# Kernel optimization log

Hardware: AMD Instinct MI355X
Metric: run time of the kernel (lower is better)

## Reference

```python
import jax, jax.numpy as jnp
import numpy as np

B, CF, HH, WW = 32, 768, 28, 28
M, NH = 32, 1024
BETA = 0.05

def _lin(key, out_d, in_d):
    k1, k2 = jax.random.split(key)
    s = 1.0 / np.sqrt(in_d)
    W = jax.random.uniform(k1, (out_d, in_d), minval=-s, maxval=s, dtype=jnp.float32)
    b = jax.random.uniform(k2, (out_d,), minval=-s, maxval=s, dtype=jnp.float32)
    return W, b

def setup_inputs() -> dict:
    key = jax.random.key(0)
    ks = jax.random.split(key, 16)
    inp = {
        'F': jax.random.normal(ks[0], (B, CF, HH, WW), dtype=jnp.float32),
        'A': jax.random.uniform(ks[1], (B, M, HH, WW), dtype=jnp.float32),
        'C': jax.random.normal(ks[2], (1, M * CF), dtype=jnp.float32),
    }
    names = ['xi', 'hi', 'xf', 'hf', 'xo', 'ho', 'xc', 'hc']
    for i, n in enumerate(names):
        in_d = CF if n[0] == 'x' else NH
        W, b = _lin(ks[3 + i], NH, in_d)
        inp['W' + n] = W
        inp['b' + n] = b
    return inp

def reference(F, A, C, Wxi, bxi, Whi, bhi, Wxf, bxf, Whf, bhf, Wxo, bxo, Who, bho, Wxc, bxc, Whc, bhc):
    b = F.shape[0]
    hw = F.shape[2] * F.shape[3]
    m = A.shape[1]
    # BAP: avg-pool of F * A_i over spatial dims, for each attention map -> [B, M, Cf]
    V = jnp.einsum('bchw,bmhw->bmc', F, A) / hw
    V = V.reshape(b, -1)  # [B, M*Cf]
    # RCLoss (center update + detached MSE)
    tmp = jnp.sum(V - C, axis=0)  # [M*Cf]
    C_new = C + (BETA * tmp / b)[None, :]
    diff = jax.lax.stop_gradient(V) - jax.lax.stop_gradient(C_new)
    rcloss = jnp.mean(diff * diff)
    # LSTM over M steps (note: original uses sigmoid for all gates via Sig_i)
    X_seq = V.reshape(b, m, -1).transpose(1, 0, 2)  # [M, B, Cf]
    h0 = jnp.zeros((b, Whi.shape[0]), dtype=V.dtype)
    c0 = jnp.zeros((b, Whi.shape[0]), dtype=V.dtype)
    def step(carry, X):
        H, Cc = carry
        I = jax.nn.sigmoid(X @ Wxi.T + bxi + H @ Whi.T + bhi)
        Fg = jax.nn.sigmoid(X @ Wxf.T + bxf + H @ Whf.T + bhf)
        O = jax.nn.sigmoid(X @ Wxo.T + bxo + H @ Who.T + bho)
        Ct = jnp.tanh(X @ Wxc.T + bxc + H @ Whc.T + bhc)
        Cc = Fg * Cc + I * Ct
        H = O * jnp.tanh(Cc)
        return (H, Cc), None
    (H, _), _ = jax.lax.scan(step, (h0, c0), X_seq)
    return (H, rcloss, C_new)
```

## Files before the change

### kernel.cpp

```cpp
#include <hip/hip_runtime.h>
#include <math.h>

#define CF 768
#define MM 32
#define HW 784
#define MCF 24576
#define BETA 0.05f

typedef __attribute__((ext_vector_type(8))) short bf16x8;
typedef __attribute__((ext_vector_type(4))) float f32x4;

__device__ __forceinline__ unsigned short bf16rne(float x) {
    unsigned int bits = __float_as_uint(x);
    unsigned int r = (bits + 0x7fffu + ((bits >> 16) & 1u)) >> 16;
    return (unsigned short)r;
}
__device__ __forceinline__ float bf2f(unsigned short u) {
    return __uint_as_float(((unsigned int)u) << 16);
}
__device__ __forceinline__ float sigf(float x) { return 1.f / (1.f + __expf(-x)); }
__device__ __forceinline__ float ftanh(float x) {
    x = fminf(fmaxf(x, -12.f), 12.f);
    float e = __expf(2.f * x);
    return (e - 1.f) / (e + 1.f);
}

__device__ __forceinline__ void cvt8(const float4 a, const float4 b, unsigned short* u) {
    u[0] = bf16rne(a.x); u[1] = bf16rne(a.y); u[2] = bf16rne(a.z); u[3] = bf16rne(a.w);
    u[4] = bf16rne(b.x); u[5] = bf16rne(b.y); u[6] = bf16rne(b.z); u[7] = bf16rne(b.w);
}

__global__ __launch_bounds__(256) void kA3M(
    const float* __restrict__ F, const float* __restrict__ Ain,
    unsigned short* __restrict__ Vbf,
    const float* __restrict__ Wxi, const float* __restrict__ Wxf,
    const float* __restrict__ Wxo, const float* __restrict__ Wxc,
    unsigned short* __restrict__ Wxbf,
    const float* __restrict__ Whi, const float* __restrict__ Whf,
    const float* __restrict__ Who, const float* __restrict__ Whc,
    unsigned short* __restrict__ Wbf,
    float* __restrict__ outRC) {
    __shared__ unsigned short Alds[3328 * 8];
    __shared__ unsigned short Flds[2][512 * 8];
    const int bid = blockIdx.x;
    const int t = threadIdx.x;

    if (bid >= 384) {
        if (bid == 384 && t == 0) outRC[0] = 0.f;
        if (bid < 1920) {
            int gid = (bid - 384) * 256 + t;
            int row = gid / 96;
            int kq = (gid - row * 96) * 8;
            int g = row >> 10, j = row & 1023;
            const float* Wg = (g == 0) ? Wxi : (g == 1) ? Wxf : (g == 2) ? Wxo : Wxc;
            const float* src = Wg + (size_t)j * CF + kq;
            float4 f0 = *(const float4*)src;
            float4 f1 = *(const float4*)(src + 4);
            unsigned short u[8];
            cvt8(f0, f1, u);
            *(uint4*)&Wxbf[(size_t)row * CF + kq] = *(const uint4*)u;
        } else {
            size_t tid8 = ((size_t)(bid - 1920) * 256 + t) * 8;
            int row = (int)(tid8 >> 10);
            int k = (int)(tid8 & 1023);
            int g = row >> 10, j = row & 1023;
            const float* Wg = (g == 0) ? Whi : (g == 1) ? Whf : (g == 2) ? Who : Whc;
            const float* src = Wg + (size_t)j * 1024 + k;
            float4 f0 = *(const float4*)src;
            float4 f1 = *(const float4*)(src + 4);
            unsigned short u[8];
            cvt8(f0, f1, u);
            *(uint4*)&Wbf[tid8] = *(const uint4*)u;
        }
        return;
    }

    const int b = bid / 12, ct = bid - b * 12;
    const int cbase = ct * 64;
    const int lane = t & 63, w = t >> 6;
    const int n = lane & 15, q = lane >> 4;

    {
        float4 va[7][2];
        #pragma unroll
        for (int it = 0; it < 7; ++it) {
            int s = it * 256 + t;
            int lf = s & 63, mk = s >> 6;
            int m = (mk & 1) * 16 + (lf & 15);
            int k = (mk >> 1) * 32 + (lf >> 4) * 8;
            if (k < 784) {
                const float* src = Ain + ((size_t)(b * 32 + m)) * 784 + k;
                va[it][0] = *(const float4*)src;
                va[it][1] = *(const float4*)(src + 4);
            } else {
                va[it][0] = (float4){0, 0, 0, 0};
                va[it][1] = (float4){0, 0, 0, 0};
            }
        }
        #pragma unroll
        for (int it = 0; it < 7; ++it) {
            int s = it * 256 + t;
            unsigned short u[8];
            cvt8(va[it][0], va[it][1], u);
            *(uint4*)&Alds[s * 8] = *(const uint4*)u;
        }
        float4 vb[6][2];
        #pragma unroll
        for (int it = 0; it < 6; ++it) {
            int s = (it + 7) * 256 + t;
            int lf = s & 63, mk = s >> 6;
            int m = (mk & 1) * 16 + (lf & 15);
            int k = (mk >> 1) * 32 + (lf >> 4) * 8;
            if (k < 784) {
                const float* src = Ain + ((size_t)(b * 32 + m)) * 784 + k;
                vb[it][0] = *(const float4*)src;
                vb[it][1] = *(const float4*)(src + 4);
            } else {
                vb[it][0] = (float4){0, 0, 0, 0};
                vb[it][1] = (float4){0, 0, 0, 0};
            }
        }
        #pragma unroll
        for (int it = 0; it < 6; ++it) {
            int s = (it + 7) * 256 + t;
            unsigned short u[8];
            cvt8(vb[it][0], vb[it][1], u);
            *(uint4*)&Alds[s * 8] = *(const uint4*)u;
        }
    }

    float4 pf[2][2];
    const int s0 = t, s1 = t + 256;
    const int ls0 = s0 & 63, kc20 = (s0 >> 6) & 1, nt0 = s0 >> 7;
    const int ls1 = s1 & 63, kc21 = (s1 >> 6) & 1, nt1 = s1 >> 7;
    const int fc0 = nt0 * 16 + (ls0 & 15), fk0 = kc20 * 32 + (ls0 >> 4) * 8;
    const int fc1 = nt1 * 16 + (ls1 & 15), fk1 = kc21 * 32 + (ls1 >> 4) * 8;
    const float* Fr0 = F + ((size_t)(b * 768) + cbase + fc0) * 784;
    const float* Fr1 = F + ((size_t)(b * 768) + cbase + fc1) * 784;
    pf[0][0] = *(const float4*)(Fr0 + fk0); pf[0][1] = *(const float4*)(Fr0 + fk0 + 4);
    pf[1][0] = *(const float4*)(Fr1 + fk1); pf[1][1] = *(const float4*)(Fr1 + fk1 + 4);
    {
        unsigned short u[8];
        cvt8(pf[0][0], pf[0][1], u); *(uint4*)&Flds[0][s0 * 8] = *(const uint4*)u;
        cvt8(pf[1][0], pf[1][1], u); *(uint4*)&Flds[0][s1 * 8] = *(const uint4*)u;
    }
    __syncthreads();

    f32x4 acc[2];
    acc[0] = (f32x4){0, 0, 0, 0};
    acc[1] = (f32x4){0, 0, 0, 0};

    for (int c13 = 0; c13 < 13; ++c13) {
        const int buf = c13 & 1;
        if (c13 < 12) {
            int k0 = (c13 + 1) * 64 + fk0;
            int k1 = (c13 + 1) * 64 + fk1;
            if (k0 < 784) {
                pf[0][0] = *(const float4*)(Fr0 + k0); pf[0][1] = *(const float4*)(Fr0 + k0 + 4);
            } else { pf[0][0] = (float4){0,0,0,0}; pf[0][1] = (float4){0,0,0,0}; }
            if (k1 < 784) {
                pf[1][0] = *(const float4*)(Fr1 + k1); pf[1][1] = *(const float4*)(Fr1 + k1 + 4);
            } else { pf[1][0] = (float4){0,0,0,0}; pf[1][1] = (float4){0,0,0,0}; }
        }
        #pragma unroll
        for (int kc2 = 0; kc2 < 2; ++kc2) {
            const int kc = c13 * 2 + kc2;
            bf16x8 bfr = *(const bf16x8*)&Flds[buf][((w * 2 + kc2) * 64 + lane) * 8];
            bf16x8 a0 = *(const bf16x8*)&Alds[((kc * 2 + 0) * 64 + lane) * 8];
            bf16x8 a1 = *(const bf16x8*)&Alds[((kc * 2 + 1) * 64 + lane) * 8];
            acc[0] = __builtin_amdgcn_mfma_f32_16x16x32_bf16(a0, bfr, acc[0], 0, 0, 0);
            acc[1] = __builtin_amdgcn_mfma_f32_16x16x32_bf16(a1, bfr, acc[1], 0, 0, 0);
        }
        if (c13 < 12) {
            unsigned short u[8];
            cvt8(pf[0][0], pf[0][1], u); *(uint4*)&Flds[buf ^ 1][s0 * 8] = *(const uint4*)u;
            cvt8(pf[1][0], pf[1][1], u); *(uint4*)&Flds[buf ^ 1][s1 * 8] = *(const uint4*)u;
        }
        __syncthreads();
    }

    #pragma unroll
    for (int mt = 0; mt < 2; ++mt)
        #pragma unroll
        for (int r = 0; r < 4; ++r)
            Vbf[(size_t)(b * 32 + mt * 16 + q * 4 + r) * 768 + cbase + w * 16 + n] =
                bf16rne(acc[mt][r] * (1.f / 784.f));
}

__global__ __launch_bounds__(512) void kC3B(
    const unsigned short* __restrict__ Vbf,
    const unsigned short* __restrict__ Wxbf,
    const float* __restrict__ bxi, const float* __restrict__ bxf,
    const float* __restrict__ bxo, const float* __restrict__ bxc,
    const float* __restrict__ bhi, const float* __restrict__ bhf,
    const float* __restrict__ bho, const float* __restrict__ bhc,
    unsigned short* __restrict__ Xbf,
    const float* __restrict__ C, float* __restrict__ Cnew_out,
    float* __restrict__ outRC) {
    __shared__ unsigned short Asg[512 * 8];
    const int bx = blockIdx.x;
    const int by = blockIdx.y;
    const int t = threadIdx.x;

    if (bx >= 16) {
        int e = (bx - 16) * 32 + by;
        if (e < 48) {
            int j = e * 512 + t;
            float c = C[j];
            float s = 0.f;
            #pragma unroll 4
            for (int b = 0; b < 32; ++b) s += bf2f(Vbf[(size_t)b * MCF + j]);
            float cn = c + BETA * (s * (1.f / 32.f) - c);
            Cnew_out[j] = cn;
            float ds = 0.f;
            #pragma unroll 4
            for (int b = 0; b < 32; ++b) {
                float d = bf2f(Vbf[(size_t)b * MCF + j]) - cn;
                ds = fmaf(d, d, ds);
            }
            float* red = (float*)Asg;
            red[t] = ds;
            __syncthreads();
            for (int off = 256; off > 0; off >>= 1) {
                if (t < off) red[t] += red[t + off];
                __syncthreads();
            }
            if (t == 0) atomicAdd(outRC, red[0] * (1.f / (32.f * 24576.f)));
        }
        return;
    }

    const int lane = t & 63;
    const int w = t >> 6;
    const int n = lane & 15;
    const int q = lane >> 4;
    const int mbase = bx * 64;

    const int st_row = (w & 3) * 16 + n;
    const int st_kb  = (w >> 2) * 4 + q;
    const int st_rg  = mbase + st_row;
    const int st_vrow = (st_rg & 31) * 32 + (st_rg >> 5);
    const unsigned short* st_src = Vbf + (size_t)st_vrow * CF + st_kb * 8;

    const int nb = by * 128 + w * 16;
    const unsigned short* Brow = Wxbf + (size_t)(nb + n) * CF + q * 8;

    f32x4 acc[4];
    #pragma unroll
    for (int g = 0; g < 4; ++g) acc[g] = (f32x4){0.f, 0.f, 0.f, 0.f};

    uint4 st = *(const uint4*)st_src;
    for (int kc = 0; kc < 12; ++kc) {
        __syncthreads();
        *(uint4*)&Asg[t * 8] = st;
        __syncthreads();
        if (kc + 1 < 12) st = *(const uint4*)(st_src + (kc + 1) * 64);
        #pragma unroll
        for (int p = 0; p < 2; ++p) {
            bf16x8 bfr = *(const bf16x8*)(Brow + kc * 64 + p * 32);
            #pragma unroll
            for (int g = 0; g < 4; ++g) {
                bf16x8 a = *(const bf16x8*)&Asg[((p * 4 + g) * 64 + lane) * 8];
                acc[g] = __builtin_amdgcn_mfma_f32_16x16x32_bf16(a, bfr, acc[g], 0, 0, 0);
            }
        }
    }

    const int gg = by >> 3;
    const int j = (by & 7) * 128 + w * 16 + n;
    const float* bx_ = (gg == 0) ? bxi : (gg == 1) ? bxf : (gg == 2) ? bxo : bxc;
    const float* bh_ = (gg == 0) ? bhi : (gg == 1) ? bhf : (gg == 2) ? bho : bhc;
    const float bias = bx_[j] + bh_[j];
    #pragma unroll
    for (int g = 0; g < 4; ++g) {
        #pragma unroll
        for (int rr = 0; rr < 4; ++rr) {
            int rg = mbase + g * 16 + q * 4 + rr;
            int tt = rg >> 5, bb = rg & 31;
            Xbf[((size_t)(tt * 4 + gg) * 32 + bb) * 1024 + j] = bf16rne(acc[g][rr] + bias);
        }
    }
}

__global__ __launch_bounds__(512) void kStep(
    const unsigned short* __restrict__ Wbf,
    const unsigned short* __restrict__ Xbf,
    const unsigned short* __restrict__ Hprev,
    unsigned short* __restrict__ Hnext,
    float* __restrict__ Cst,
    float* __restrict__ outH,
    int step) {
    __shared__ float pbuf[8][32][17];
    __shared__ float sbuf[32][17];
    const int bi = blockIdx.x;
    const int jbase = bi * 4;
    const int t = threadIdx.x;
    const int lane = t & 63;
    const int w = t >> 6;
    const int n = lane & 15;
    const int q = lane >> 4;

    const int pb = t >> 4, pnn = t & 15;
    const int pg = pnn >> 2, pjj = pnn & 3;
    const float xv = bf2f(Xbf[(((size_t)step * 4 + pg) * 32 + pb) * 1024 + jbase + pjj]);
    float cprev = 0.f;
    if (step > 0 && t < 128) cprev = Cst[(t >> 2) * 1024 + jbase + (t & 3)];

    if (step > 0) {
        const int g = n >> 2, jj = n & 3;
        const unsigned short* Wrow = Wbf + ((size_t)(g * 1024 + jbase + jj)) * 1024 + w * 128;
        const unsigned short* hb0 = Hprev + (size_t)n * 1024 + w * 128;
        const unsigned short* hb1 = Hprev + (size_t)(n + 16) * 1024 + w * 128;
        f32x4 acc0 = {0.f, 0.f, 0.f, 0.f};
        f32x4 acc1 = {0.f, 0.f, 0.f, 0.f};
        #pragma unroll
        for (int ks = 0; ks < 4; ++ks) {
            int k = ks * 32 + q * 8;
            bf16x8 bfrag = *(const bf16x8*)(Wrow + k);
            bf16x8 a0 = *(const bf16x8*)(hb0 + k);
            bf16x8 a1 = *(const bf16x8*)(hb1 + k);
            acc0 = __builtin_amdgcn_mfma_f32_16x16x32_bf16(a0, bfrag, acc0, 0, 0, 0);
            acc1 = __builtin_amdgcn_mfma_f32_16x16x32_bf16(a1, bfrag, acc1, 0, 0, 0);
        }
        #pragma unroll
        for (int r = 0; r < 4; ++r) {
            pbuf[w][q * 4 + r][n] = acc0[r];
            pbuf[w][16 + q * 4 + r][n] = acc1[r];
        }
    }
    __syncthreads();
    {
        float s = xv;
        if (step > 0) {
            #pragma unroll
            for (int w2 = 0; w2 < 8; ++w2) s += pbuf[w2][pb][pnn];
        }
        sbuf[pb][pnn] = s;
    }
    __syncthreads();
    if (t < 128) {
        int b = t >> 2, jj = t & 3;
        float I  = sigf(sbuf[b][jj]);
        float Fg = sigf(sbuf[b][4 + jj]);
        float O  = sigf(sbuf[b][8 + jj]);
        float Ct = ftanh(sbuf[b][12 + jj]);
        float c = fmaf(Fg, cprev, I * Ct);
        Cst[b * 1024 + jbase + jj] = c;
        float h = O * ftanh(c);
        if (step < 31) {
            Hnext[b * 1024 + jbase + jj] = bf16rne(h);
        } else {
            outH[b * 1024 + jbase + jj] = h;
        }
    }
}

extern "C" void kernel_launch(void* const* d_in, const int* in_sizes, int n_in,
                              void* d_out, int out_size, void* d_ws, size_t ws_size,
                              hipStream_t stream) {
    const float* F   = (const float*)d_in[0];
    const float* A   = (const float*)d_in[1];
    const float* C   = (const float*)d_in[2];
    const float* Wxi = (const float*)d_in[3];
    const float* bxi = (const float*)d_in[4];
    const float* Whi = (const float*)d_in[5];
    const float* bhi = (const float*)d_in[6];
    const float* Wxf = (const float*)d_in[7];
    const float* bxf = (const float*)d_in[8];
    const float* Whf = (const float*)d_in[9];
    const float* bhf = (const float*)d_in[10];
    const float* Wxo = (const float*)d_in[11];
    const float* bxo = (const float*)d_in[12];
    const float* Who = (const float*)d_in[13];
    const float* bho = (const float*)d_in[14];
    const float* Wxc = (const float*)d_in[15];
    const float* bxc = (const float*)d_in[16];
    const float* Whc = (const float*)d_in[17];
    const float* bhc = (const float*)d_in[18];

    float* out   = (float*)d_out;
    float* outH  = out;
    float* outRC = out + 32768;
    float* outC  = out + 32769;

    float* ws = (float*)d_ws;
    unsigned short* Xbf  = (unsigned short*)ws;
    unsigned short* Wxbf = (unsigned short*)(ws + 2097152);
    unsigned short* Wbf  = (unsigned short*)(ws + 3670016);
    unsigned short* Vbf  = (unsigned short*)(ws + 5767168);
    unsigned short* Hbf  = (unsigned short*)(ws + 6160384);
    float* Cst  = ws + 6193152;

    kA3M<<<dim3(3968), 256, 0, stream>>>(F, A, Vbf,
                                         Wxi, Wxf, Wxo, Wxc, Wxbf,
                                         Whi, Whf, Who, Whc, Wbf, outRC);
    kC3B<<<dim3(18, 32), 512, 0, stream>>>(Vbf, Wxbf,
                                           bxi, bxf, bxo, bxc,
                                           bhi, bhf, bho, bhc, Xbf,
                                           C, outC, outRC);

    for (int step = 0; step < 32; ++step) {
        const unsigned short* Hprev = Hbf + ((step + 1) & 1) * 32768;
        unsigned short* Hnext = (unsigned short*)(Hbf + (step & 1) * 32768);
        kStep<<<dim3(256), 512, 0, stream>>>(Wbf, Xbf, Hprev, Hnext, Cst, outH, step);
    }
}
```

Baseline: 234.4 us.

## Load BAP MFMA fragments directly from global with split-K across waves

The BAP einsum kernel no longer stages A and F tiles through LDS with double buffering. Each wave now loads its bf16 MFMA fragments straight from global memory, and the K dimension is split between wave pairs, with partial sums combined through a small LDS buffer. Channel tiles shrink from 64 to 32, which doubles the block count for more parallelism and removes the per-iteration barriers. The cost is that A fragments are reloaded per block and per wave with uncoalesced 32-byte row reads instead of coming from a shared LDS copy.

Measured after the change: 236.4 us. About the same (+0.9%).

```diff
diff --git a/kernel.cpp b/kernel.cpp
--- a/kernel.cpp
+++ b/kernel.cpp
@@ -29,8 +29,16 @@
     u[0] = bf16rne(a.x); u[1] = bf16rne(a.y); u[2] = bf16rne(a.z); u[3] = bf16rne(a.w);
     u[4] = bf16rne(b.x); u[5] = bf16rne(b.y); u[6] = bf16rne(b.z); u[7] = bf16rne(b.w);
 }
-
-__global__ __launch_bounds__(256) void kA3M(
+__device__ __forceinline__ bf16x8 ld_frag(const float* p, bool valid) {
+    float4 lo, hi;
+    if (valid) { lo = *(const float4*)p; hi = *(const float4*)(p + 4); }
+    else { lo = (float4){0,0,0,0}; hi = (float4){0,0,0,0}; }
+    unsigned short u[8];
+    cvt8(lo, hi, u);
+    return *(const bf16x8*)u;
+}
+
+__global__ __launch_bounds__(256) void kFE(
     const float* __restrict__ F, const float* __restrict__ Ain,
     unsigned short* __restrict__ Vbf,
     const float* __restrict__ Wxi, const float* __restrict__ Wxf,
@@ -40,15 +48,14 @@
     const float* __restrict__ Who, const float* __restrict__ Whc,
     unsigned short* __restrict__ Wbf,
     float* __restrict__ outRC) {
-    __shared__ unsigned short Alds[3328 * 8];
-    __shared__ unsigned short Flds[2][512 * 8];
+    __shared__ float pls[2][2][64][4];
     const int bid = blockIdx.x;
     const int t = threadIdx.x;
 
-    if (bid >= 384) {
-        if (bid == 384 && t == 0) outRC[0] = 0.f;
-        if (bid < 1920) {
-            int gid = (bid - 384) * 256 + t;
+    if (bid >= 768) {
+        if (bid == 768 && t == 0) outRC[0] = 0.f;
+        if (bid < 2304) {
+            int gid = (bid - 768) * 256 + t;
             int row = gid / 96;
             int kq = (gid - row * 96) * 8;
             int g = row >> 10, j = row & 1023;
@@ -60,7 +67,7 @@
             cvt8(f0, f1, u);
             *(uint4*)&Wxbf[(size_t)row * CF + kq] = *(const uint4*)u;
         } else {
-            size_t tid8 = ((size_t)(bid - 1920) * 256 + t) * 8;
+            size_t tid8 = ((size_t)(bid - 2304) * 256 + t) * 8;
             int row = (int)(tid8 >> 10);
             int k = (int)(tid8 & 1023);
             int g = row >> 10, j = row & 1023;
@@ -75,116 +82,54 @@
         return;
     }
 
-    const int b = bid / 12, ct = bid - b * 12;
-    const int cbase = ct * 64;
+    const int b = bid / 24, ct = bid - b * 24;
+    const int cbase = ct * 32;
     const int lane = t & 63, w = t >> 6;
+    const int cw = w & 1, kh = w >> 1;
     const int n = lane & 15, q = lane >> 4;
 
-    {
-        float4 va[7][2];
-        #pragma unroll
-        for (int it = 0; it < 7; ++it) {
-            int s = it * 256 + t;
-            int lf = s & 63, mk = s >> 6;
-            int m = (mk & 1) * 16 + (lf & 15);
-            int k = (mk >> 1) * 32 + (lf >> 4) * 8;
-            if (k < 784) {
-                const float* src = Ain + ((size_t)(b * 32 + m)) * 784 + k;
-                va[it][0] = *(const float4*)src;
-                va[it][1] = *(const float4*)(src + 4);
-            } else {
-                va[it][0] = (float4){0, 0, 0, 0};
-                va[it][1] = (float4){0, 0, 0, 0};
-            }
-        }
-        #pragma unroll
-        for (int it = 0; it < 7; ++it) {
-            int s = it * 256 + t;
-            unsigned short u[8];
-            cvt8(va[it][0], va[it][1], u);
-            *(uint4*)&Alds[s * 8] = *(const uint4*)u;
-        }
-        float4 vb[6][2];
-        #pragma unroll
-        for (int it = 0; it < 6; ++it) {
-            int s = (it + 7) * 256 + t;
-            int lf = s & 63, mk = s >> 6;
-            int m = (mk & 1) * 16 + (lf & 15);
-            int k = (mk >> 1) * 32 + (lf >> 4) * 8;
-            if (k < 784) {
-                const float* src = Ain + ((size_t)(b * 32 + m)) * 784 + k;
-                vb[it][0] = *(const float4*)src;
-                vb[it][1] = *(const float4*)(src + 4);
-            } else {
-                vb[it][0] = (float4){0, 0, 0, 0};
-                vb[it][1] = (float4){0, 0, 0, 0};
-            }
-        }
-        #pragma unroll
-        for (int it = 0; it < 6; ++it) {
-            int s = (it + 7) * 256 + t;
-            unsigned short u[8];
-            cvt8(vb[it][0], vb[it][1], u);
-            *(uint4*)&Alds[s * 8] = *(const uint4*)u;
-        }
-    }
-
-    float4 pf[2][2];
-    const int s0 = t, s1 = t + 256;
-    const int ls0 = s0 & 63, kc20 = (s0 >> 6) & 1, nt0 = s0 >> 7;
-    const int ls1 = s1 & 63, kc21 = (s1 >> 6) & 1, nt1 = s1 >> 7;
-    const int fc0 = nt0 * 16 + (ls0 & 15), fk0 = kc20 * 32 + (ls0 >> 4) * 8;
-    const int fc1 = nt1 * 16 + (ls1 & 15), fk1 = kc21 * 32 + (ls1 >> 4) * 8;
-    const float* Fr0 = F + ((size_t)(b * 768) + cbase + fc0) * 784;
-    const float* Fr1 = F + ((size_t)(b * 768) + cbase + fc1) * 784;
-    pf[0][0] = *(const float4*)(Fr0 + fk0); pf[0][1] = *(const float4*)(Fr0 + fk0 + 4);
-    pf[1][0] = *(const float4*)(Fr1 + fk1); pf[1][1] = *(const float4*)(Fr1 + fk1 + 4);
-    {
-        unsigned short u[8];
-        cvt8(pf[0][0], pf[0][1], u); *(uint4*)&Flds[0][s0 * 8] = *(const uint4*)u;
-        cvt8(pf[1][0], pf[1][1], u); *(uint4*)&Flds[0][s1 * 8] = *(const uint4*)u;
+    const float* Arow0 = Ain + ((size_t)(b * 32 + n)) * HW;
+    const float* Arow1 = Ain + ((size_t)(b * 32 + 16 + n)) * HW;
+    const float* Frow  = F + ((size_t)(b * CF) + cbase + cw * 16 + n) * HW;
+    const int kq8 = q * 8;
+
+    f32x4 acc0 = {0.f, 0.f, 0.f, 0.f};
+    f32x4 acc1 = {0.f, 0.f, 0.f, 0.f};
+
+    #pragma unroll 4
+    for (int kc = 0; kc < 13; ++kc) {
+        const int k = (kh * 13 + kc) * 32 + kq8;
+        const bool valid = (k < HW);
+        bf16x8 bf_ = ld_frag(Frow + k, valid);
+        bf16x8 a0 = ld_frag(Arow0 + k, valid);
+        bf16x8 a1 = ld_frag(Arow1 + k, valid);
+        acc0 = __builtin_amdgcn_mfma_f32_16x16x32_bf16(a0, bf_, acc0, 0, 0, 0);
+        acc1 = __builtin_amdgcn_mfma_f32_16x16x32_bf16(a1, bf_, acc1, 0, 0, 0);
+    }
+
+    if (kh == 1) {
+        #pragma unroll
+        for (int r = 0; r < 4; ++r) {
+            pls[cw][0][lane][r] = acc0[r];
+            pls[cw][1][lane][r] = acc1[r];
+        }
     }
     __syncthreads();
-
-    f32x4 acc[2];
-    acc[0] = (f32x4){0, 0, 0, 0};
-    acc[1] = (f32x4){0, 0, 0, 0};
-
-    for (int c13 = 0; c13 < 13; ++c13) {
-        const int buf = c13 & 1;
-        if (c13 < 12) {
-            int k0 = (c13 + 1) * 64 + fk0;
-            int k1 = (c13 + 1) * 64 + fk1;
-            if (k0 < 784) {
-                pf[0][0] = *(const float4*)(Fr0 + k0); pf[0][1] = *(const float4*)(Fr0 + k0 + 4);
-            } else { pf[0][0] = (float4){0,0,0,0}; pf[0][1] = (float4){0,0,0,0}; }
-            if (k1 < 784) {
-                pf[1][0] = *(const float4*)(Fr1 + k1); pf[1][1] = *(const float4*)(Fr1 + k1 + 4);
-            } else { pf[1][0] = (float4){0,0,0,0}; pf[1][1] = (float4){0,0,0,0}; }
-        }
-        #pragma unroll
-        for (int kc2 = 0; kc2 < 2; ++kc2) {
-            const int kc = c13 * 2 + kc2;
-            bf16x8 bfr = *(const bf16x8*)&Flds[buf][((w * 2 + kc2) * 64 + lane) * 8];
-            bf16x8 a0 = *(const bf16x8*)&Alds[((kc * 2 + 0) * 64 + lane) * 8];
-            bf16x8 a1 = *(const bf16x8*)&Alds[((kc * 2 + 1) * 64 + lane) * 8];
-            acc[0] = __builtin_amdgcn_mfma_f32_16x16x32_bf16(a0, bfr, acc[0], 0, 0, 0);
-            acc[1] = __builtin_amdgcn_mfma_f32_16x16x32_bf16(a1, bfr, acc[1], 0, 0, 0);
-        }
-        if (c13 < 12) {
-            unsigned short u[8];
-            cvt8(pf[0][0], pf[0][1], u); *(uint4*)&Flds[buf ^ 1][s0 * 8] = *(const uint4*)u;
-            cvt8(pf[1][0], pf[1][1], u); *(uint4*)&Flds[buf ^ 1][s1 * 8] = *(const uint4*)u;
-        }
-        __syncthreads();
-    }
-
-    #pragma unroll
-    for (int mt = 0; mt < 2; ++mt)
-        #pragma unroll
-        for (int r = 0; r < 4; ++r)
-            Vbf[(size_t)(b * 32 + mt * 16 + q * 4 + r) * 768 + cbase + w * 16 + n] =
-                bf16rne(acc[mt][r] * (1.f / 784.f));
+    if (kh == 0) {
+        #pragma unroll
+        for (int r = 0; r < 4; ++r) {
+            acc0[r] += pls[cw][0][lane][r];
+            acc1[r] += pls[cw][1][lane][r];
+        }
+        #pragma unroll
+        for (int r = 0; r < 4; ++r) {
+            int m0 = q * 4 + r;
+            Vbf[(size_t)(b * 32 + m0) * CF + cbase + cw * 16 + n] =
+                bf16rne(acc0[r] * (1.f / 784.f));
+            Vbf[(size_t)(b * 32 + 16 + m0) * CF + cbase + cw * 16 + n] =
+                bf16rne(acc1[r] * (1.f / 784.f));
+        }
+    }
 }
 
 __global__ __launch_bounds__(512) void kC3B(
@@ -391,9 +336,9 @@
     unsigned short* Hbf  = (unsigned short*)(ws + 6160384);
     float* Cst  = ws + 6193152;
 
-    kA3M<<<dim3(3968), 256, 0, stream>>>(F, A, Vbf,
-                                         Wxi, Wxf, Wxo, Wxc, Wxbf,
-                                         Whi, Whf, Who, Whc, Wbf, outRC);
+    kFE<<<dim3(4352), 256, 0, stream>>>(F, A, Vbf,
+                                        Wxi, Wxf, Wxo, Wxc, Wxbf,
+                                        Whi, Whf, Who, Whc, Wbf, outRC);
     kC3B<<<dim3(18, 32), 512, 0, stream>>>(Vbf, Wxbf,
                                            bxi, bxf, bxo, bxc,
                                            bhi, bhf, bho, bhc, Xbf,
```
